# Optimization experiments

Measured on AMD Instinct MI355X. Metric: run time of the kernel, lower is better.

Reference implementation:

```python
import jax, jax.numpy as jnp
import numpy as np

N = 6144       # nodes
E = 12288      # edges (~2N for a sparse simplicial complex)
NF = 32        # node features
EF = 16        # edge features
NH = [32, 32]  # node_hidden
EH = [16, 16]  # edge_hidden
EPS = 1e-5


def setup_inputs() -> dict:
    key = jax.random.key(0)
    ks = jax.random.split(key, 24)
    s = 0.1  # weight init scale
    inp = {}
    inp["X_n"] = jax.random.normal(ks[0], (N, NF), jnp.float32)
    inp["X_e"] = jax.random.normal(ks[1], (E, EF), jnp.float32)
    # normalized adjacency-like operator (non-negative, row mass ~1)
    inp["A_tilde"] = jax.random.uniform(ks[2], (N, N), jnp.float32) * (1.0 / N)
    # normalized Hodge-1 Laplacian-like operator
    inp["L1_tilde"] = jax.random.normal(ks[3], (E, E), jnp.float32) * (1.0 / np.sqrt(E))
    # incidence-like operator
    inp["B1"] = jax.random.normal(ks[4], (N, E), jnp.float32) * (1.0 / np.sqrt(E))
    # GNN linear layers: weight [out, in] (torch convention)
    inp["gnn_W0"] = jax.random.normal(ks[5], (NH[0], NF), jnp.float32) * s
    inp["gnn_b0"] = jnp.zeros((NH[0],), jnp.float32)
    inp["gnn_W1"] = jax.random.normal(ks[6], (NH[1], NH[0]), jnp.float32) * s
    inp["gnn_b1"] = jnp.zeros((NH[1],), jnp.float32)
    # HoSC layer 0: theta in=EF out=EH[0], BN params
    inp["th_W0"] = jax.random.normal(ks[7], (EH[0], EF), jnp.float32) * s
    inp["th_b0"] = jnp.zeros((EH[0],), jnp.float32)
    inp["bn_g0"] = jnp.ones((EH[0],), jnp.float32)
    inp["bn_b0"] = jnp.zeros((EH[0],), jnp.float32)
    # HoSC layer 1: input collapses to 1 channel (max keepdim)
    inp["th_W1"] = jax.random.normal(ks[8], (EH[1], 1), jnp.float32) * s
    inp["th_b1"] = jnp.zeros((EH[1],), jnp.float32)
    inp["bn_g1"] = jnp.ones((EH[1],), jnp.float32)
    inp["bn_b1"] = jnp.zeros((EH[1],), jnp.float32)
    # head: fc1 in = NH[-1] + len(EH) = 34, out = 2N; fc2 out = 1
    inp["fc1_W"] = jax.random.normal(ks[9], (2 * N, NH[-1] + len(EH)), jnp.float32) * s
    inp["fc1_b"] = jnp.zeros((2 * N,), jnp.float32)
    inp["fc2_W"] = jax.random.normal(ks[10], (1, 2 * N), jnp.float32) * s
    inp["fc2_b"] = jnp.zeros((1,), jnp.float32)
    return inp


def _gnn_layer(A, H, W, b):
    # H <- relu((A @ H) @ W^T + b)
    return jax.nn.relu(jnp.matmul(jnp.matmul(A, H), W.T) + b)


def _hosc_layer(Z, L1, W, b, g, beta):
    Zt = jnp.matmul(Z, W.T) + b            # theta
    Zc = jnp.matmul(L1, Zt)                # Laplacian conv
    m = jnp.mean(Zc, axis=0)               # BatchNorm1d (training-mode batch stats)
    v = jnp.var(Zc, axis=0)
    Zp = jax.nn.relu(g * (Zc - m) * jax.lax.rsqrt(v + EPS) + beta)
    return jnp.max(Zp, axis=1, keepdims=True)  # [E, 1]


def reference(X_n, X_e, A_tilde, L1_tilde, B1,
              gnn_W0, gnn_b0, gnn_W1, gnn_b1,
              th_W0, th_b0, bn_g0, bn_b0,
              th_W1, th_b1, bn_g1, bn_b1,
              fc1_W, fc1_b, fc2_W, fc2_b):
    # GNN over nodes
    H = _gnn_layer(A_tilde, X_n, gnn_W0, gnn_b0)
    H_n = _gnn_layer(A_tilde, H, gnn_W1, gnn_b1)      # [N, NH[-1]]
    # HoSC over edges
    Z0 = _hosc_layer(X_e, L1_tilde, th_W0, th_b0, bn_g0, bn_b0)  # [E, 1]
    Z1 = _hosc_layer(Z0, L1_tilde, th_W1, th_b1, bn_g1, bn_b1)   # [E, 1]
    Z_cat = jnp.concatenate([Z0, Z1], axis=1)         # [E, 2]
    H_e = jnp.matmul(B1, Z_cat)                       # [N, 2]
    # head
    Hcat = jnp.concatenate([H_n, H_e], axis=1)        # [N, 34]
    f = jax.nn.relu(jnp.matmul(Hcat, fc1_W.T) + fc1_b)
    f = jnp.matmul(f, fc2_W.T) + fc2_b                # [N, 1]
    return jax.nn.sigmoid(f).squeeze(-1)              # [N]
```

## Files before the change

kernel.cpp:

```cpp
#include <hip/hip_runtime.h>
#include <hip/hip_bf16.h>
#include <math.h>

#define NND 6144
#define NED 12288
static constexpr float EPS_BN = 1e-5f;

#define HN_OFF    0
#define HE_OFF    196608
#define ST_OFF    208896
#define Y_OFF     208960
#define T0_OFF    405568
#define T1_OFF    602176
#define Z0_OFF    798784
#define Z1_OFF    811072
#define U_OFF     823360
#define S_OFF     835648
#define PP_OFF    847936

typedef float floatx4 __attribute__((ext_vector_type(4)));

__device__ __forceinline__ float4 ntload4(const float* p) {
  floatx4 v = __builtin_nontemporal_load(reinterpret_cast<const floatx4*>(p));
  return make_float4(v.x, v.y, v.z, v.w);
}
__device__ __forceinline__ float4 ld4(const float* p) {
  return *reinterpret_cast<const float4*>(p);
}

__device__ __forceinline__ void gll16(const float* g, float* l) {
  __builtin_amdgcn_global_load_lds(
      (const __attribute__((address_space(1))) unsigned int*)g,
      (__attribute__((address_space(3))) unsigned int*)l, 16, 0, 0);
}

__global__ void init_ws(float* __restrict__ p, int n) {
  int i = blockIdx.x * blockDim.x + threadIdx.x;
  if (i < n) p[i] = 0.f;
}

template<int IC, int OC>
__global__ void small_mm_T(const float* __restrict__ X, const float* __restrict__ W,
                           const float* __restrict__ bias, float* __restrict__ CT, int M) {
  int m = blockIdx.x * blockDim.x + threadIdx.x;
  if (m >= M) return;
  float x[IC];
  #pragma unroll
  for (int k = 0; k < IC; k += 4) {
    float4 v = ld4(X + (size_t)m * IC + k);
    x[k] = v.x; x[k+1] = v.y; x[k+2] = v.z; x[k+3] = v.w;
  }
  #pragma unroll
  for (int oc = 0; oc < OC; ++oc) {
    float s = bias ? bias[oc] : 0.f;
    #pragma unroll
    for (int k = 0; k < IC; ++k) s = fmaf(x[k], W[oc * IC + k], s);
    CT[(size_t)oc * M + m] = s;
  }
}

template<int NC, int CG, bool RELU, bool STATS>
__global__ __launch_bounds__(256, 2)
void gemm_pipe(const float* __restrict__ A, const float* __restrict__ YT,
               const float* __restrict__ bias, float* __restrict__ out,
               float* __restrict__ stats, int K) {
  constexpr int RG = 4 / CG;
  constexpr int ROWS = RG * 4;
  constexpr int YR_W = NC / 4;
  constexpr int AR_W = ROWS / 4;
  constexpr int G = YR_W + AR_W;
  __shared__ float Yb[2][NC][256];
  __shared__ float Ab[2][ROWS][256];
  __shared__ float sst[32];

  const int tid = threadIdx.x;
  const int lane = tid & 63;
  const int w = tid >> 6;
  const int cg = w % CG, rg = w / CG;
  const int r0 = blockIdx.x * ROWS;
  const int c0 = cg * 16;

  auto stage = [&](int kb, int b) {
    #pragma unroll
    for (int i = 0; i < YR_W; ++i) {
      const int yr = w * YR_W + i;
      gll16(YT + (size_t)yr * K + kb + lane * 4, &Yb[b][yr][0]);
    }
    #pragma unroll
    for (int i = 0; i < AR_W; ++i) {
      const int ar = w * AR_W + i;
      gll16(A + (size_t)(r0 + ar) * K + kb + lane * 4, &Ab[b][ar][0]);
    }
  };

  float acc[4][16];
  #pragma unroll
  for (int r = 0; r < 4; ++r)
    #pragma unroll
    for (int c = 0; c < 16; ++c) acc[r][c] = 0.f;

  stage(0, 0);
  stage(256, 1);
  asm volatile("s_waitcnt vmcnt(%0)" :: "n"(G) : "memory");
  __builtin_amdgcn_sched_barrier(0);
  __builtin_amdgcn_s_barrier();

  int cur = 0;
  for (int kb = 0; kb < K; kb += 256) {
    float4 av[4];
    #pragma unroll
    for (int r = 0; r < 4; ++r)
      av[r] = *reinterpret_cast<const float4*>(&Ab[cur][rg * 4 + r][lane * 4]);
    #pragma unroll
    for (int c = 0; c < 16; ++c) {
      const float4 y = *reinterpret_cast<const float4*>(&Yb[cur][c0 + c][lane * 4]);
      #pragma unroll
      for (int r = 0; r < 4; ++r) {
        acc[r][c] = fmaf(av[r].x, y.x, acc[r][c]);
        acc[r][c] = fmaf(av[r].y, y.y, acc[r][c]);
        acc[r][c] = fmaf(av[r].z, y.z, acc[r][c]);
        acc[r][c] = fmaf(av[r].w, y.w, acc[r][c]);
      }
    }
    __builtin_amdgcn_s_barrier();
    if (kb + 512 < K) {
      stage(kb + 512, cur);
      asm volatile("s_waitcnt vmcnt(%0)" :: "n"(G) : "memory");
    } else {
      asm volatile("s_waitcnt vmcnt(0)" ::: "memory");
    }
    __builtin_amdgcn_sched_barrier(0);
    __builtin_amdgcn_s_barrier();
    cur ^= 1;
  }

  float wv[64];
  #pragma unroll
  for (int r = 0; r < 4; ++r)
    #pragma unroll
    for (int c = 0; c < 16; ++c) wv[r * 16 + c] = acc[r][c];
  #pragma unroll
  for (int b = 5; b >= 0; --b) {
    const int m = 1 << b;
    const bool hi = (lane & m) != 0;
    #pragma unroll
    for (int i = 0; i < (1 << b); ++i) {
      float a  = wv[i];
      float bb = wv[i + (1 << b)];
      float send = hi ? a : bb;
      float recv = __shfl_xor(send, m, 64);
      wv[i] = (hi ? bb : a) + recv;
    }
  }

  const int rsel = lane >> 4, csel = lane & 15;
  const int rw = rg * 4;
  float v = wv[0] + (bias ? bias[c0 + csel] : 0.f);
  if (RELU) v = fmaxf(v, 0.f);
  out[(size_t)(r0 + rw + rsel) * NC + c0 + csel] = v;

  if (STATS) {
    if (tid < 32) sst[tid] = 0.f;
    __syncthreads();
    float sv = v, qv = v * v;
    sv += __shfl_xor(sv, 16, 64); sv += __shfl_xor(sv, 32, 64);
    qv += __shfl_xor(qv, 16, 64); qv += __shfl_xor(qv, 32, 64);
    if (lane < 16) { atomicAdd(&sst[csel], sv); atomicAdd(&sst[16 + csel], qv); }
    __syncthreads();
    if (tid < 32) atomicAdd(stats + tid, sst[tid]);
  }
}

template<int MODE, bool REV>
__global__ __launch_bounds__(256)
void rowpass(const float* __restrict__ Mt, const float* __restrict__ za,
             const float* __restrict__ zb, float* __restrict__ o1,
             float* __restrict__ o2, int K) {
  const int lane = threadIdx.x & 63;
  const int blk = REV ? (gridDim.x - 1 - blockIdx.x) : blockIdx.x;
  const int row = blk * 4 + (threadIdx.x >> 6);
  const float* mp = Mt + (size_t)row * K;
  float accA = 0.f, accB = 0.f;
  float4 a0 = ntload4(mp + lane * 4);
  float4 a1 = ntload4(mp + 256 + lane * 4);
  float4 z0 = ld4(za + lane * 4);
  float4 z1 = ld4(za + 256 + lane * 4);
  float4 y0, y1;
  if (MODE == 1) { y0 = ld4(zb + lane * 4); y1 = ld4(zb + 256 + lane * 4); }
  for (int kb = 0; kb < K; kb += 512) {
    const int k = kb + lane * 4;
    const bool more = (kb + 512) < K;
    float4 na0, na1, nz0, nz1, ny0, ny1;
    if (more) {
      na0 = ntload4(mp + k + 512);
      na1 = ntload4(mp + k + 768);
      nz0 = ld4(za + k + 512);
      nz1 = ld4(za + k + 768);
      if (MODE == 1) { ny0 = ld4(zb + k + 512); ny1 = ld4(zb + k + 768); }
    }
    if (MODE == 0) {
      accA += a0.x*z0.x + a0.y*z0.y + a0.z*z0.z + a0.w*z0.w
            + a1.x*z1.x + a1.y*z1.y + a1.z*z1.z + a1.w*z1.w;
      accB += a0.x + a0.y + a0.z + a0.w + a1.x + a1.y + a1.z + a1.w;
    } else {
      accA += a0.x*z0.x + a0.y*z0.y + a0.z*z0.z + a0.w*z0.w
            + a1.x*z1.x + a1.y*z1.y + a1.z*z1.z + a1.w*z1.w;
      accB += a0.x*y0.x + a0.y*y0.y + a0.z*y0.z + a0.w*y0.w
            + a1.x*y1.x + a1.y*y1.y + a1.z*y1.z + a1.w*y1.w;
    }
    if (more) {
      a0 = na0; a1 = na1; z0 = nz0; z1 = nz1;
      if (MODE == 1) { y0 = ny0; y1 = ny1; }
    }
  }
  #pragma unroll
  for (int m = 1; m < 64; m <<= 1) {
    accA += __shfl_xor(accA, m, 64);
    accB += __shfl_xor(accB, m, 64);
  }
  if (lane == 0) {
    if (MODE == 0) { o1[row] = accA; o2[row] = accB; }
    else { o1[row * 2] = accA; o1[row * 2 + 1] = accB; }
  }
}

__global__ void bn_max(const float* __restrict__ Zc, const float* __restrict__ stats,
                       const float* __restrict__ g, const float* __restrict__ beta,
                       float* __restrict__ Z, int E) {
  const int e = blockIdx.x * blockDim.x + threadIdx.x;
  if (e >= E) return;
  const float invE = 1.f / (float)E;
  float best = -3.4e38f;
  #pragma unroll
  for (int c = 0; c < 16; ++c) {
    float m = stats[c] * invE;
    float var = stats[16 + c] * invE - m * m;
    float sc = g[c] * rsqrtf(var + EPS_BN);
    float sh = beta[c] - m * sc;
    float x = Zc[(size_t)e * 16 + c];
    best = fmaxf(best, fmaf(x, sc, sh));
  }
  Z[e] = fmaxf(best, 0.f);
}

__global__ void us_stats(const float* __restrict__ u, const float* __restrict__ s,
                         float* __restrict__ st5) {
  const int e = blockIdx.x * 256 + threadIdx.x;
  const int lane = threadIdx.x & 63;
  const int w = threadIdx.x >> 6;
  const float uu = u[e], ss = s[e];
  float v[5] = {uu, ss, uu * uu, ss * ss, uu * ss};
  #pragma unroll
  for (int i = 0; i < 5; ++i)
    #pragma unroll
    for (int m = 1; m < 64; m <<= 1) v[i] += __shfl_xor(v[i], m, 64);
  __shared__ float red[4][5];
  if (lane == 0) {
    #pragma unroll
    for (int i = 0; i < 5; ++i) red[w][i] = v[i];
  }
  __syncthreads();
  if (threadIdx.x < 5) {
    float t = red[0][threadIdx.x] + red[1][threadIdx.x] + red[2][threadIdx.x] + red[3][threadIdx.x];
    atomicAdd(st5 + threadIdx.x, t);
  }
}

__global__ void z1_from_us(const float* __restrict__ u, const float* __restrict__ s,
                           const float* __restrict__ st5,
                           const float* __restrict__ W1, const float* __restrict__ b1,
                           const float* __restrict__ g, const float* __restrict__ beta,
                           float* __restrict__ Z1, int E) {
  const int e = blockIdx.x * blockDim.x + threadIdx.x;
  if (e >= E) return;
  const float invE = 1.f / (float)E;
  const float Su = st5[0], Ss = st5[1], Suu = st5[2], Sss = st5[3], Sus = st5[4];
  const float uu = u[e], ssv = s[e];
  float best = -3.4e38f;
  #pragma unroll
  for (int c = 0; c < 16; ++c) {
    const float wc = W1[c], bc = b1[c];
    const float mean = (wc * Su + bc * Ss) * invE;
    const float ex2 = (wc * wc * Suu + 2.f * wc * bc * Sus + bc * bc * Sss) * invE;
    const float var = ex2 - mean * mean;
    const float sc = g[c] * rsqrtf(var + EPS_BN);
    const float sh = beta[c] - mean * sc;
    best = fmaxf(best, fmaf(wc * uu + bc * ssv, sc, sh));
  }
  Z1[e] = fmaxf(best, 0.f);
}

__global__ __launch_bounds__(256, 2)
void head(const float* __restrict__ Hn, const float* __restrict__ he,
          const float* __restrict__ W1, const float* __restrict__ b1,
          const float* __restrict__ w2, float* __restrict__ prepart) {
  const int t = threadIdx.x;
  const int nb = blockIdx.x;
  const int jb = blockIdx.y;
  int n[3];
  float h[3][34];
  float acc[3] = {0.f, 0.f, 0.f};
  #pragma unroll
  for (int i = 0; i < 3; ++i) {
    n[i] = nb * 768 + i * 256 + t;
    #pragma unroll
    for (int k = 0; k < 32; k += 4) {
      float4 v = ld4(Hn + (size_t)n[i] * 32 + k);
      h[i][k] = v.x; h[i][k+1] = v.y; h[i][k+2] = v.z; h[i][k+3] = v.w;
    }
    float2 e2 = *reinterpret_cast<const float2*>(he + n[i] * 2);
    h[i][32] = e2.x;
    h[i][33] = e2.y;
  }
  const int j0 = jb * 192;
  for (int j = j0; j < j0 + 192; ++j) {
    const float* wp = W1 + (size_t)j * 34;
    const float bj = b1[j], vj = w2[j];
    float s0 = bj, s1 = bj, s2 = bj;
    #pragma unroll
    for (int k = 0; k < 34; ++k) {
      const float wk = wp[k];
      s0 = fmaf(h[0][k], wk, s0);
      s1 = fmaf(h[1][k], wk, s1);
      s2 = fmaf(h[2][k], wk, s2);
    }
    acc[0] += fmaxf(s0, 0.f) * vj;
    acc[1] += fmaxf(s1, 0.f) * vj;
    acc[2] += fmaxf(s2, 0.f) * vj;
  }
  #pragma unroll
  for (int i = 0; i < 3; ++i) prepart[(size_t)jb * NND + n[i]] = acc[i];
}

__global__ void final_k(const float* __restrict__ pp, const float* __restrict__ b2,
                        float* __restrict__ out, int Nn) {
  const int i = blockIdx.x * blockDim.x + threadIdx.x;
  if (i >= Nn) return;
  float s = 0.f;
  #pragma unroll
  for (int j = 0; j < 64; ++j) s += pp[(size_t)j * NND + i];
  out[i] = 1.f / (1.f + expf(-(s + b2[0])));
}

extern "C" void kernel_launch(void* const* d_in, const int* in_sizes, int n_in,
                              void* d_out, int out_size, void* d_ws, size_t ws_size,
                              hipStream_t stream) {
  const float* X_n   = (const float*)d_in[0];
  const float* X_e   = (const float*)d_in[1];
  const float* A     = (const float*)d_in[2];
  const float* L1    = (const float*)d_in[3];
  const float* B1    = (const float*)d_in[4];
  const float* gW0   = (const float*)d_in[5];
  const float* gb0   = (const float*)d_in[6];
  const float* gW1   = (const float*)d_in[7];
  const float* gb1   = (const float*)d_in[8];
  const float* tW0   = (const float*)d_in[9];
  const float* tb0   = (const float*)d_in[10];
  const float* bng0  = (const float*)d_in[11];
  const float* bnb0  = (const float*)d_in[12];
  const float* tW1   = (const float*)d_in[13];
  const float* tb1   = (const float*)d_in[14];
  const float* bng1  = (const float*)d_in[15];
  const float* bnb1  = (const float*)d_in[16];
  const float* fc1W  = (const float*)d_in[17];
  const float* fc1b  = (const float*)d_in[18];
  const float* fc2W  = (const float*)d_in[19];
  const float* fc2b  = (const float*)d_in[20];

  float* ws   = (float*)d_ws;
  float* Hn   = ws + HN_OFF;
  float* he   = ws + HE_OFF;
  float* st   = ws + ST_OFF;
  float* Y    = ws + Y_OFF;
  float* T0   = ws + T0_OFF;
  float* T1   = ws + T1_OFF;
  float* Z0   = ws + Z0_OFF;
  float* Z1   = ws + Z1_OFF;
  float* u    = ws + U_OFF;
  float* s    = ws + S_OFF;
  float* pp   = ws + PP_OFF;
  float* out  = (float*)d_out;

  init_ws<<<1, 64, 0, stream>>>(st, 64);

  small_mm_T<32, 32><<<24, 256, 0, stream>>>(X_n, gW0, nullptr, Y, NND);
  gemm_pipe<32, 2, true, false><<<768, 256, 0, stream>>>(A, Y, gb0, T0, nullptr, NND);
  small_mm_T<32, 32><<<24, 256, 0, stream>>>(T0, gW1, nullptr, Y, NND);
  gemm_pipe<32, 2, true, false><<<768, 256, 0, stream>>>(A, Y, gb1, Hn, nullptr, NND);

  small_mm_T<16, 16><<<48, 256, 0, stream>>>(X_e, tW0, tb0, T1, NED);
  gemm_pipe<16, 1, false, true><<<768, 256, 0, stream>>>(L1, T1, nullptr, T0, st, NED);
  bn_max<<<48, 256, 0, stream>>>(T0, st, bng0, bnb0, Z0, NED);

  rowpass<0, true><<<3072, 256, 0, stream>>>(L1, Z0, nullptr, u, s, NED);
  us_stats<<<48, 256, 0, stream>>>(u, s, st + 32);
  z1_from_us<<<48, 256, 0, stream>>>(u, s, st + 32, tW1, tb1, bng1, bnb1, Z1, NED);

  rowpass<1, false><<<1536, 256, 0, stream>>>(B1, Z0, Z1, he, nullptr, NED);

  head<<<dim3(8, 64), 256, 0, stream>>>(Hn, he, fc1W, fc1b, fc2W, pp);
  final_k<<<24, 256, 0, stream>>>(pp, fc2b, out, NND);
}
```

Measured before the change: 659.5 us.

## Replace LDS-staged pipelined GEMM with register-only per-wave row GEMM

Measured after the change: 878.7 us. 1.33x slower.

```diff
diff --git a/kernel.cpp b/kernel.cpp
--- a/kernel.cpp
+++ b/kernel.cpp
@@ -28,12 +28,6 @@
   return *reinterpret_cast<const float4*>(p);
 }
 
-__device__ __forceinline__ void gll16(const float* g, float* l) {
-  __builtin_amdgcn_global_load_lds(
-      (const __attribute__((address_space(1))) unsigned int*)g,
-      (__attribute__((address_space(3))) unsigned int*)l, 16, 0, 0);
-}
-
 __global__ void init_ws(float* __restrict__ p, int n) {
   int i = blockIdx.x * blockDim.x + threadIdx.x;
   if (i < n) p[i] = 0.f;
@@ -59,115 +53,105 @@
   }
 }
 
-template<int NC, int CG, bool RELU, bool STATS>
-__global__ __launch_bounds__(256, 2)
-void gemm_pipe(const float* __restrict__ A, const float* __restrict__ YT,
+template<int NC, bool RELU, bool STATS>
+__global__ __launch_bounds__(256)
+void gemm_rows(const float* __restrict__ A, const float* __restrict__ YT,
                const float* __restrict__ bias, float* __restrict__ out,
                float* __restrict__ stats, int K) {
-  constexpr int RG = 4 / CG;
-  constexpr int ROWS = RG * 4;
-  constexpr int YR_W = NC / 4;
-  constexpr int AR_W = ROWS / 4;
-  constexpr int G = YR_W + AR_W;
-  __shared__ float Yb[2][NC][256];
-  __shared__ float Ab[2][ROWS][256];
-  __shared__ float sst[32];
-
-  const int tid = threadIdx.x;
-  const int lane = tid & 63;
-  const int w = tid >> 6;
-  const int cg = w % CG, rg = w / CG;
-  const int r0 = blockIdx.x * ROWS;
-  const int c0 = cg * 16;
-
-  auto stage = [&](int kb, int b) {
-    #pragma unroll
-    for (int i = 0; i < YR_W; ++i) {
-      const int yr = w * YR_W + i;
-      gll16(YT + (size_t)yr * K + kb + lane * 4, &Yb[b][yr][0]);
-    }
-    #pragma unroll
-    for (int i = 0; i < AR_W; ++i) {
-      const int ar = w * AR_W + i;
-      gll16(A + (size_t)(r0 + ar) * K + kb + lane * 4, &Ab[b][ar][0]);
-    }
-  };
-
-  float acc[4][16];
-  #pragma unroll
-  for (int r = 0; r < 4; ++r)
-    #pragma unroll
-    for (int c = 0; c < 16; ++c) acc[r][c] = 0.f;
-
-  stage(0, 0);
-  stage(256, 1);
-  asm volatile("s_waitcnt vmcnt(%0)" :: "n"(G) : "memory");
-  __builtin_amdgcn_sched_barrier(0);
-  __builtin_amdgcn_s_barrier();
-
-  int cur = 0;
+  const int lane = threadIdx.x & 63;
+  const int w = threadIdx.x >> 6;
+  const int rows0 = (blockIdx.x * 4 + w) * 3;
+
+  const float* ap[3];
+  #pragma unroll
+  for (int r = 0; r < 3; ++r) ap[r] = A + (size_t)(rows0 + r) * K;
+
+  float acc[3][NC];
+  #pragma unroll
+  for (int r = 0; r < 3; ++r)
+    #pragma unroll
+    for (int c = 0; c < NC; ++c) acc[r][c] = 0.f;
+
+  float4 a[3], an[3];
+  #pragma unroll
+  for (int r = 0; r < 3; ++r) a[r] = ld4(ap[r] + lane * 4);
+
   for (int kb = 0; kb < K; kb += 256) {
-    float4 av[4];
-    #pragma unroll
-    for (int r = 0; r < 4; ++r)
-      av[r] = *reinterpret_cast<const float4*>(&Ab[cur][rg * 4 + r][lane * 4]);
-    #pragma unroll
-    for (int c = 0; c < 16; ++c) {
-      const float4 y = *reinterpret_cast<const float4*>(&Yb[cur][c0 + c][lane * 4]);
+    const int k = kb + lane * 4;
+    const bool more = (kb + 256) < K;
+    if (more) {
       #pragma unroll
-      for (int r = 0; r < 4; ++r) {
-        acc[r][c] = fmaf(av[r].x, y.x, acc[r][c]);
-        acc[r][c] = fmaf(av[r].y, y.y, acc[r][c]);
-        acc[r][c] = fmaf(av[r].z, y.z, acc[r][c]);
-        acc[r][c] = fmaf(av[r].w, y.w, acc[r][c]);
+      for (int r = 0; r < 3; ++r) an[r] = ld4(ap[r] + k + 256);
+    }
+    #pragma unroll
+    for (int c = 0; c < NC; ++c) {
+      const float4 y = ld4(YT + (size_t)c * K + k);
+      #pragma unroll
+      for (int r = 0; r < 3; ++r) {
+        acc[r][c] = fmaf(a[r].x, y.x, acc[r][c]);
+        acc[r][c] = fmaf(a[r].y, y.y, acc[r][c]);
+        acc[r][c] = fmaf(a[r].z, y.z, acc[r][c]);
+        acc[r][c] = fmaf(a[r].w, y.w, acc[r][c]);
       }
     }
-    __builtin_amdgcn_s_barrier();
-    if (kb + 512 < K) {
-      stage(kb + 512, cur);
-      asm volatile("s_waitcnt vmcnt(%0)" :: "n"(G) : "memory");
-    } else {
-      asm volatile("s_waitcnt vmcnt(0)" ::: "memory");
-    }
-    __builtin_amdgcn_sched_barrier(0);
-    __builtin_amdgcn_s_barrier();
-    cur ^= 1;
-  }
-
-  float wv[64];
-  #pragma unroll
-  for (int r = 0; r < 4; ++r)
-    #pragma unroll
-    for (int c = 0; c < 16; ++c) wv[r * 16 + c] = acc[r][c];
-  #pragma unroll
-  for (int b = 5; b >= 0; --b) {
-    const int m = 1 << b;
-    const bool hi = (lane & m) != 0;
-    #pragma unroll
-    for (int i = 0; i < (1 << b); ++i) {
-      float a  = wv[i];
-      float bb = wv[i + (1 << b)];
-      float send = hi ? a : bb;
-      float recv = __shfl_xor(send, m, 64);
-      wv[i] = (hi ? bb : a) + recv;
-    }
-  }
-
-  const int rsel = lane >> 4, csel = lane & 15;
-  const int rw = rg * 4;
-  float v = wv[0] + (bias ? bias[c0 + csel] : 0.f);
-  if (RELU) v = fmaxf(v, 0.f);
-  out[(size_t)(r0 + rw + rsel) * NC + c0 + csel] = v;
+    if (more) {
+      #pragma unroll
+      for (int r = 0; r < 3; ++r) a[r] = an[r];
+    }
+  }
+
+  #pragma unroll
+  for (int r = 0; r < 3; ++r)
+    #pragma unroll
+    for (int c = 0; c < NC; ++c) {
+      acc[r][c] += __shfl_xor(acc[r][c], 32, 64);
+      if (NC == 16) acc[r][c] += __shfl_xor(acc[r][c], 16, 64);
+    }
+
+  constexpr int LB = (NC == 16) ? 4 : 5;
+  float rowv[3];
+  #pragma unroll
+  for (int r = 0; r < 3; ++r) {
+    float wv[NC];
+    #pragma unroll
+    for (int c = 0; c < NC; ++c) wv[c] = acc[r][c];
+    #pragma unroll
+    for (int b = LB - 1; b >= 0; --b) {
+      const int m = 1 << b;
+      const bool hi = (lane & m) != 0;
+      #pragma unroll
+      for (int i = 0; i < (1 << b); ++i) {
+        float x  = wv[i];
+        float yy = wv[i + (1 << b)];
+        float send = hi ? x : yy;
+        float recv = __shfl_xor(send, m, 64);
+        wv[i] = (hi ? yy : x) + recv;
+      }
+    }
+    rowv[r] = wv[0];
+  }
+
+  const int csel = lane & (NC - 1);
+  if (lane < NC) {
+    #pragma unroll
+    for (int r = 0; r < 3; ++r) {
+      float v = rowv[r] + (bias ? bias[csel] : 0.f);
+      if (RELU) v = fmaxf(v, 0.f);
+      out[(size_t)(rows0 + r) * NC + csel] = v;
+    }
+  }
 
   if (STATS) {
-    if (tid < 32) sst[tid] = 0.f;
+    __shared__ float sst[32];
+    if (threadIdx.x < 32) sst[threadIdx.x] = 0.f;
     __syncthreads();
-    float sv = v, qv = v * v;
-    sv += __shfl_xor(sv, 16, 64); sv += __shfl_xor(sv, 32, 64);
-    qv += __shfl_xor(qv, 16, 64); qv += __shfl_xor(qv, 32, 64);
-    if (lane < 16) { atomicAdd(&sst[csel], sv); atomicAdd(&sst[16 + csel], qv); }
+    if (lane < 16) {
+      const float v0 = rowv[0], v1 = rowv[1], v2 = rowv[2];
+      atomicAdd(&sst[csel & 15], v0 + v1 + v2);
+      atomicAdd(&sst[16 + (csel & 15)], v0 * v0 + v1 * v1 + v2 * v2);
+    }
     __syncthreads();
-    if (tid < 32) atomicAdd(stats + tid, sst[tid]);
+    if (threadIdx.x < 32) atomicAdd(stats + threadIdx.x, sst[threadIdx.x]);
   }
 }
 
@@ -384,12 +368,12 @@
   init_ws<<<1, 64, 0, stream>>>(st, 64);
 
   small_mm_T<32, 32><<<24, 256, 0, stream>>>(X_n, gW0, nullptr, Y, NND);
-  gemm_pipe<32, 2, true, false><<<768, 256, 0, stream>>>(A, Y, gb0, T0, nullptr, NND);
+  gemm_rows<32, true, false><<<512, 256, 0, stream>>>(A, Y, gb0, T0, nullptr, NND);
   small_mm_T<32, 32><<<24, 256, 0, stream>>>(T0, gW1, nullptr, Y, NND);
-  gemm_pipe<32, 2, true, false><<<768, 256, 0, stream>>>(A, Y, gb1, Hn, nullptr, NND);
+  gemm_rows<32, true, false><<<512, 256, 0, stream>>>(A, Y, gb1, Hn, nullptr, NND);
 
   small_mm_T<16, 16><<<48, 256, 0, stream>>>(X_e, tW0, tb0, T1, NED);
-  gemm_pipe<16, 1, false, true><<<768, 256, 0, stream>>>(L1, T1, nullptr, T0, st, NED);
+  gemm_rows<16, false, true><<<1024, 256, 0, stream>>>(L1, T1, nullptr, T0, st, NED);
   bn_max<<<48, 256, 0, stream>>>(T0, st, bng0, bnb0, Z0, NED);
 
   rowpass<0, true><<<3072, 256, 0, stream>>>(L1, Z0, nullptr, u, s, NED);
```

## Load A directly to registers in GEMM, two rows per wave in rowpass, fuse stats

Applied to the files above, without the earlier changes.

Result: faster. 624.5 us (-5.3%).

```diff
diff --git a/kernel.cpp b/kernel.cpp
--- a/kernel.cpp
+++ b/kernel.cpp
@@ -34,14 +34,11 @@
       (__attribute__((address_space(3))) unsigned int*)l, 16, 0, 0);
 }
 
-__global__ void init_ws(float* __restrict__ p, int n) {
-  int i = blockIdx.x * blockDim.x + threadIdx.x;
-  if (i < n) p[i] = 0.f;
-}
-
-template<int IC, int OC>
+template<int IC, int OC, bool ZEROST>
 __global__ void small_mm_T(const float* __restrict__ X, const float* __restrict__ W,
-                           const float* __restrict__ bias, float* __restrict__ CT, int M) {
+                           const float* __restrict__ bias, float* __restrict__ CT,
+                           float* __restrict__ zst, int M) {
+  if (ZEROST && blockIdx.x == 0 && threadIdx.x < 64) zst[threadIdx.x] = 0.f;
   int m = blockIdx.x * blockDim.x + threadIdx.x;
   if (m >= M) return;
   float x[IC];
@@ -60,18 +57,13 @@
 }
 
 template<int NC, int CG, bool RELU, bool STATS>
-__global__ __launch_bounds__(256, 2)
-void gemm_pipe(const float* __restrict__ A, const float* __restrict__ YT,
-               const float* __restrict__ bias, float* __restrict__ out,
-               float* __restrict__ stats, int K) {
-  constexpr int RG = 4 / CG;
-  constexpr int ROWS = RG * 4;
-  constexpr int YR_W = NC / 4;
-  constexpr int AR_W = ROWS / 4;
-  constexpr int G = YR_W + AR_W;
-  __shared__ float Yb[2][NC][256];
-  __shared__ float Ab[2][ROWS][256];
-  __shared__ float sst[32];
+__global__ __launch_bounds__(256)
+void gemm_g(const float* __restrict__ A, const float* __restrict__ YT,
+            const float* __restrict__ bias, float* __restrict__ out,
+            float* __restrict__ stats, int K) {
+  constexpr int ROWS = (4 / CG) * 4;
+  constexpr int GPW = NC * 2 / 4;
+  __shared__ float Yb[NC][512];
 
   const int tid = threadIdx.x;
   const int lane = tid & 63;
@@ -80,58 +72,65 @@
   const int r0 = blockIdx.x * ROWS;
   const int c0 = cg * 16;
 
-  auto stage = [&](int kb, int b) {
-    #pragma unroll
-    for (int i = 0; i < YR_W; ++i) {
-      const int yr = w * YR_W + i;
-      gll16(YT + (size_t)yr * K + kb + lane * 4, &Yb[b][yr][0]);
-    }
-    #pragma unroll
-    for (int i = 0; i < AR_W; ++i) {
-      const int ar = w * AR_W + i;
-      gll16(A + (size_t)(r0 + ar) * K + kb + lane * 4, &Ab[b][ar][0]);
+  const float* ap[4];
+  #pragma unroll
+  for (int r = 0; r < 4; ++r) ap[r] = A + (size_t)(r0 + rg * 4 + r) * K;
+
+  auto stage = [&](int kb) {
+    #pragma unroll
+    for (int i = 0; i < GPW; ++i) {
+      const int f = w * GPW + i;
+      const int row = f >> 1, half = f & 1;
+      gll16(YT + (size_t)row * K + kb + half * 256 + lane * 4,
+            &Yb[row][half * 256]);
     }
   };
 
+  float4 av[4][2], av2[4][2];
+  auto loadA = [&](int kb, float4 (*dst)[2]) {
+    #pragma unroll
+    for (int r = 0; r < 4; ++r)
+      #pragma unroll
+      for (int s = 0; s < 2; ++s)
+        dst[r][s] = ld4(ap[r] + kb + s * 256 + lane * 4);
+  };
+
   float acc[4][16];
   #pragma unroll
   for (int r = 0; r < 4; ++r)
     #pragma unroll
     for (int c = 0; c < 16; ++c) acc[r][c] = 0.f;
 
-  stage(0, 0);
-  stage(256, 1);
-  asm volatile("s_waitcnt vmcnt(%0)" :: "n"(G) : "memory");
-  __builtin_amdgcn_sched_barrier(0);
-  __builtin_amdgcn_s_barrier();
-
-  int cur = 0;
-  for (int kb = 0; kb < K; kb += 256) {
-    float4 av[4];
-    #pragma unroll
-    for (int r = 0; r < 4; ++r)
-      av[r] = *reinterpret_cast<const float4*>(&Ab[cur][rg * 4 + r][lane * 4]);
-    #pragma unroll
-    for (int c = 0; c < 16; ++c) {
-      const float4 y = *reinterpret_cast<const float4*>(&Yb[cur][c0 + c][lane * 4]);
+  stage(0);
+  loadA(0, av);
+  __syncthreads();
+
+  for (int kb = 0; kb < K; kb += 512) {
+    #pragma unroll
+    for (int s = 0; s < 2; ++s)
+      #pragma unroll
+      for (int c = 0; c < 16; ++c) {
+        const float4 y = *reinterpret_cast<const float4*>(&Yb[c0 + c][s * 256 + lane * 4]);
+        #pragma unroll
+        for (int r = 0; r < 4; ++r) {
+          acc[r][c] = fmaf(av[r][s].x, y.x, acc[r][c]);
+          acc[r][c] = fmaf(av[r][s].y, y.y, acc[r][c]);
+          acc[r][c] = fmaf(av[r][s].z, y.z, acc[r][c]);
+          acc[r][c] = fmaf(av[r][s].w, y.w, acc[r][c]);
+        }
+      }
+    const bool more = (kb + 512) < K;
+    __syncthreads();
+    if (more) {
+      stage(kb + 512);
+      loadA(kb + 512, av2);
+      __syncthreads();
       #pragma unroll
       for (int r = 0; r < 4; ++r) {
-        acc[r][c] = fmaf(av[r].x, y.x, acc[r][c]);
-        acc[r][c] = fmaf(av[r].y, y.y, acc[r][c]);
-        acc[r][c] = fmaf(av[r].z, y.z, acc[r][c]);
-        acc[r][c] = fmaf(av[r].w, y.w, acc[r][c]);
+        av[r][0] = av2[r][0];
+        av[r][1] = av2[r][1];
       }
     }
-    __builtin_amdgcn_s_barrier();
-    if (kb + 512 < K) {
-      stage(kb + 512, cur);
-      asm volatile("s_waitcnt vmcnt(%0)" :: "n"(G) : "memory");
-    } else {
-      asm volatile("s_waitcnt vmcnt(0)" ::: "memory");
-    }
-    __builtin_amdgcn_sched_barrier(0);
-    __builtin_amdgcn_s_barrier();
-    cur ^= 1;
   }
 
   float wv[64];
@@ -154,12 +153,12 @@
   }
 
   const int rsel = lane >> 4, csel = lane & 15;
-  const int rw = rg * 4;
   float v = wv[0] + (bias ? bias[c0 + csel] : 0.f);
   if (RELU) v = fmaxf(v, 0.f);
-  out[(size_t)(r0 + rw + rsel) * NC + c0 + csel] = v;
+  out[(size_t)(r0 + rg * 4 + rsel) * NC + c0 + csel] = v;
 
   if (STATS) {
+    __shared__ float sst[32];
     if (tid < 32) sst[tid] = 0.f;
     __syncthreads();
     float sv = v, qv = v * v;
@@ -173,54 +172,80 @@
 
 template<int MODE, bool REV>
 __global__ __launch_bounds__(256)
-void rowpass(const float* __restrict__ Mt, const float* __restrict__ za,
-             const float* __restrict__ zb, float* __restrict__ o1,
-             float* __restrict__ o2, int K) {
+void rowpass2(const float* __restrict__ Mt, const float* __restrict__ za,
+              const float* __restrict__ zb, float* __restrict__ o1,
+              float* __restrict__ o2, float* __restrict__ st5, int K) {
   const int lane = threadIdx.x & 63;
+  const int w = threadIdx.x >> 6;
   const int blk = REV ? (gridDim.x - 1 - blockIdx.x) : blockIdx.x;
-  const int row = blk * 4 + (threadIdx.x >> 6);
-  const float* mp = Mt + (size_t)row * K;
-  float accA = 0.f, accB = 0.f;
-  float4 a0 = ntload4(mp + lane * 4);
-  float4 a1 = ntload4(mp + 256 + lane * 4);
-  float4 z0 = ld4(za + lane * 4);
-  float4 z1 = ld4(za + 256 + lane * 4);
+  const int rA = blk * 8 + w * 2;
+  const float* mpA = Mt + (size_t)rA * K;
+  const float* mpB = mpA + K;
+  float uA = 0.f, vA = 0.f, uB = 0.f, vB = 0.f;
+
+  float4 a0A = ntload4(mpA + lane * 4), a1A = ntload4(mpA + 256 + lane * 4);
+  float4 a0B = ntload4(mpB + lane * 4), a1B = ntload4(mpB + 256 + lane * 4);
+  float4 z0 = ld4(za + lane * 4), z1 = ld4(za + 256 + lane * 4);
   float4 y0, y1;
   if (MODE == 1) { y0 = ld4(zb + lane * 4); y1 = ld4(zb + 256 + lane * 4); }
+
   for (int kb = 0; kb < K; kb += 512) {
     const int k = kb + lane * 4;
     const bool more = (kb + 512) < K;
-    float4 na0, na1, nz0, nz1, ny0, ny1;
+    float4 n0A, n1A, n0B, n1B, nz0, nz1, ny0, ny1;
     if (more) {
-      na0 = ntload4(mp + k + 512);
-      na1 = ntload4(mp + k + 768);
-      nz0 = ld4(za + k + 512);
-      nz1 = ld4(za + k + 768);
+      n0A = ntload4(mpA + k + 512); n1A = ntload4(mpA + k + 768);
+      n0B = ntload4(mpB + k + 512); n1B = ntload4(mpB + k + 768);
+      nz0 = ld4(za + k + 512);      nz1 = ld4(za + k + 768);
       if (MODE == 1) { ny0 = ld4(zb + k + 512); ny1 = ld4(zb + k + 768); }
     }
+    uA += a0A.x*z0.x + a0A.y*z0.y + a0A.z*z0.z + a0A.w*z0.w
+        + a1A.x*z1.x + a1A.y*z1.y + a1A.z*z1.z + a1A.w*z1.w;
+    uB += a0B.x*z0.x + a0B.y*z0.y + a0B.z*z0.z + a0B.w*z0.w
+        + a1B.x*z1.x + a1B.y*z1.y + a1B.z*z1.z + a1B.w*z1.w;
     if (MODE == 0) {
-      accA += a0.x*z0.x + a0.y*z0.y + a0.z*z0.z + a0.w*z0.w
-            + a1.x*z1.x + a1.y*z1.y + a1.z*z1.z + a1.w*z1.w;
-      accB += a0.x + a0.y + a0.z + a0.w + a1.x + a1.y + a1.z + a1.w;
+      vA += a0A.x + a0A.y + a0A.z + a0A.w + a1A.x + a1A.y + a1A.z + a1A.w;
+      vB += a0B.x + a0B.y + a0B.z + a0B.w + a1B.x + a1B.y + a1B.z + a1B.w;
     } else {
-      accA += a0.x*z0.x + a0.y*z0.y + a0.z*z0.z + a0.w*z0.w
-            + a1.x*z1.x + a1.y*z1.y + a1.z*z1.z + a1.w*z1.w;
-      accB += a0.x*y0.x + a0.y*y0.y + a0.z*y0.z + a0.w*y0.w
-            + a1.x*y1.x + a1.y*y1.y + a1.z*y1.z + a1.w*y1.w;
+      vA += a0A.x*y0.x + a0A.y*y0.y + a0A.z*y0.z + a0A.w*y0.w
+          + a1A.x*y1.x + a1A.y*y1.y + a1A.z*y1.z + a1A.w*y1.w;
+      vB += a0B.x*y0.x + a0B.y*y0.y + a0B.z*y0.z + a0B.w*y0.w
+          + a1B.x*y1.x + a1B.y*y1.y + a1B.z*y1.z + a1B.w*y1.w;
     }
     if (more) {
-      a0 = na0; a1 = na1; z0 = nz0; z1 = nz1;
+      a0A = n0A; a1A = n1A; a0B = n0B; a1B = n1B; z0 = nz0; z1 = nz1;
       if (MODE == 1) { y0 = ny0; y1 = ny1; }
     }
   }
   #pragma unroll
   for (int m = 1; m < 64; m <<= 1) {
-    accA += __shfl_xor(accA, m, 64);
-    accB += __shfl_xor(accB, m, 64);
+    uA += __shfl_xor(uA, m, 64); vA += __shfl_xor(vA, m, 64);
+    uB += __shfl_xor(uB, m, 64); vB += __shfl_xor(vB, m, 64);
   }
   if (lane == 0) {
-    if (MODE == 0) { o1[row] = accA; o2[row] = accB; }
-    else { o1[row * 2] = accA; o1[row * 2 + 1] = accB; }
+    if (MODE == 0) {
+      o1[rA] = uA; o2[rA] = vA;
+      o1[rA + 1] = uB; o2[rA + 1] = vB;
+    } else {
+      o1[rA * 2] = uA;     o1[rA * 2 + 1] = vA;
+      o1[rA * 2 + 2] = uB; o1[rA * 2 + 3] = vB;
+    }
+  }
+  if (MODE == 0) {
+    __shared__ float red[4][5];
+    if (lane == 0) {
+      red[w][0] = uA + uB;
+      red[w][1] = vA + vB;
+      red[w][2] = uA * uA + uB * uB;
+      red[w][3] = vA * vA + vB * vB;
+      red[w][4] = uA * vA + uB * vB;
+    }
+    __syncthreads();
+    if (threadIdx.x < 5) {
+      float t = red[0][threadIdx.x] + red[1][threadIdx.x]
+              + red[2][threadIdx.x] + red[3][threadIdx.x];
+      atomicAdd(st5 + threadIdx.x, t);
+    }
   }
 }
 
@@ -241,29 +266,6 @@
     best = fmaxf(best, fmaf(x, sc, sh));
   }
   Z[e] = fmaxf(best, 0.f);
-}
-
-__global__ void us_stats(const float* __restrict__ u, const float* __restrict__ s,
-                         float* __restrict__ st5) {
-  const int e = blockIdx.x * 256 + threadIdx.x;
-  const int lane = threadIdx.x & 63;
-  const int w = threadIdx.x >> 6;
-  const float uu = u[e], ss = s[e];
-  float v[5] = {uu, ss, uu * uu, ss * ss, uu * ss};
-  #pragma unroll
-  for (int i = 0; i < 5; ++i)
-    #pragma unroll
-    for (int m = 1; m < 64; m <<= 1) v[i] += __shfl_xor(v[i], m, 64);
-  __shared__ float red[4][5];
-  if (lane == 0) {
-    #pragma unroll
-    for (int i = 0; i < 5; ++i) red[w][i] = v[i];
-  }
-  __syncthreads();
-  if (threadIdx.x < 5) {
-    float t = red[0][threadIdx.x] + red[1][threadIdx.x] + red[2][threadIdx.x] + red[3][threadIdx.x];
-    atomicAdd(st5 + threadIdx.x, t);
-  }
 }
 
 __global__ void z1_from_us(const float* __restrict__ u, const float* __restrict__ s,
@@ -381,22 +383,19 @@
   float* pp   = ws + PP_OFF;
   float* out  = (float*)d_out;
 
-  init_ws<<<1, 64, 0, stream>>>(st, 64);
-
-  small_mm_T<32, 32><<<24, 256, 0, stream>>>(X_n, gW0, nullptr, Y, NND);
-  gemm_pipe<32, 2, true, false><<<768, 256, 0, stream>>>(A, Y, gb0, T0, nullptr, NND);
-  small_mm_T<32, 32><<<24, 256, 0, stream>>>(T0, gW1, nullptr, Y, NND);
-  gemm_pipe<32, 2, true, false><<<768, 256, 0, stream>>>(A, Y, gb1, Hn, nullptr, NND);
-
-  small_mm_T<16, 16><<<48, 256, 0, stream>>>(X_e, tW0, tb0, T1, NED);
-  gemm_pipe<16, 1, false, true><<<768, 256, 0, stream>>>(L1, T1, nullptr, T0, st, NED);
+  small_mm_T<32, 32, false><<<24, 256, 0, stream>>>(X_n, gW0, nullptr, Y, nullptr, NND);
+  gemm_g<32, 2, true, false><<<768, 256, 0, stream>>>(A, Y, gb0, T0, nullptr, NND);
+  small_mm_T<32, 32, false><<<24, 256, 0, stream>>>(T0, gW1, nullptr, Y, nullptr, NND);
+  gemm_g<32, 2, true, false><<<768, 256, 0, stream>>>(A, Y, gb1, Hn, nullptr, NND);
+
+  small_mm_T<16, 16, true><<<48, 256, 0, stream>>>(X_e, tW0, tb0, T1, st, NED);
+  gemm_g<16, 1, false, true><<<768, 256, 0, stream>>>(L1, T1, nullptr, T0, st, NED);
   bn_max<<<48, 256, 0, stream>>>(T0, st, bng0, bnb0, Z0, NED);
 
-  rowpass<0, true><<<3072, 256, 0, stream>>>(L1, Z0, nullptr, u, s, NED);
-  us_stats<<<48, 256, 0, stream>>>(u, s, st + 32);
+  rowpass2<0, true><<<1536, 256, 0, stream>>>(L1, Z0, nullptr, u, s, st + 32, NED);
   z1_from_us<<<48, 256, 0, stream>>>(u, s, st + 32, tW1, tb1, bng1, bnb1, Z1, NED);
 
-  rowpass<1, false><<<1536, 256, 0, stream>>>(B1, Z0, Z1, he, nullptr, NED);
+  rowpass2<1, false><<<768, 256, 0, stream>>>(B1, Z0, Z1, he, nullptr, nullptr, NED);
 
   head<<<dim3(8, 64), 256, 0, stream>>>(Hn, he, fc1W, fc1b, fc2W, pp);
   final_k<<<24, 256, 0, stream>>>(pp, fc2b, out, NND);
```
